# Performance work log

Measured on AMD Instinct MI355X. Metric: run time of the kernel, lower is better.

## Reference

```python
import jax, jax.numpy as jnp
import numpy as np

T, WQ, WS, C, H, W = 2, 75, 25, 640, 10, 10
WAY, SHOT = 5, 5
HID = C // 16
SCALE_VALUE = 30.0
ATTEN_SCALE_VALUE = 50.0
FROM_VALUE = 0.5
VALUE_INTERVAL = 0.3
BN_EPS = 1e-5
NORM_EPS = 1e-12


def _leaky(x):
    return jnp.where(x >= 0, x, 0.2 * x)


def _l2norm(x, axis):
    n = jnp.sqrt(jnp.sum(x * x, axis=axis, keepdims=True))
    return x / jnp.maximum(n, NORM_EPS)


def _embed(x, W_conv, bn_gamma, bn_beta, bn_mean, bn_var):
    # 1x1 conv (no bias) + eval-mode BatchNorm + LeakyReLU(0.2)
    # x: [t, n, c, h, w] -> [t, n, c, h, w]
    y = jnp.einsum('oc,tnchw->tnohw', W_conv, x)
    inv = bn_gamma / jnp.sqrt(bn_var + BN_EPS)
    y = y * inv[:, None, None] + (bn_beta - bn_mean * inv)[:, None, None]
    return _leaky(y)


def setup_inputs() -> dict:
    key = jax.random.key(0)
    ks = jax.random.split(key, 5)
    return {
        'query_feat': jax.random.normal(ks[0], (T, WQ, C, H, W), dtype=jnp.float32),
        'support_feat': jax.random.normal(ks[1], (T, WS, C, H, W), dtype=jnp.float32),
        'W_conv': jax.random.normal(ks[2], (C, C), dtype=jnp.float32) * 0.02,
        'bn_gamma': jnp.ones((C,), jnp.float32),
        'bn_beta': jnp.zeros((C,), jnp.float32),
        'bn_mean': jnp.zeros((C,), jnp.float32),
        'bn_var': jnp.ones((C,), jnp.float32),
        'psi_w1': jax.random.normal(ks[3], (C, HID), dtype=jnp.float32) * 0.04,
        'psi_b1': jnp.zeros((HID,), jnp.float32),
        'psi_w2': jax.random.normal(ks[4], (HID, 1), dtype=jnp.float32) * 0.15,
        'psi_b2': jnp.zeros((1,), jnp.float32),
        'way_num': WAY,
        'shot_num': SHOT,
    }


def reference(query_feat, support_feat, W_conv, bn_gamma, bn_beta, bn_mean, bn_var,
              psi_w1, psi_b1, psi_w2, psi_b2, way_num, shot_num):
    t, wq, c, h, w = query_feat.shape
    ws = support_feat.shape[1]
    hw = h * w

    # embedded + normalized features for the gated branch
    w_query = _embed(query_feat, W_conv, bn_gamma, bn_beta, bn_mean, bn_var)
    w_query = w_query.reshape(t, wq, c, hw).transpose(0, 1, 3, 2)      # [t, wq, hw, c]
    w_support = _embed(support_feat, W_conv, bn_gamma, bn_beta, bn_mean, bn_var)
    w_support = w_support.reshape(t, ws, c, hw).transpose(0, 2, 1, 3).reshape(t, c, ws * hw)
    w_query = _l2norm(w_query, axis=3)
    w_support = _l2norm(w_support, axis=1)

    # cosine similarity of embedded features: [t, wq, hw, ws*hw]
    f_x = jnp.einsum('tqpc,tck->tqpk', w_query, w_support)

    # AEAModule: per-location adaptive threshold from f_psi MLP
    hid = _leaky(w_query @ psi_w1 + psi_b1)                            # [t, wq, hw, HID]
    clamp_value = jax.nn.sigmoid(hid @ psi_w2 + psi_b2) * VALUE_INTERVAL + FROM_VALUE
    clamp_fx = jax.nn.sigmoid(ATTEN_SCALE_VALUE * (f_x - clamp_value))
    atten_score = clamp_fx / jnp.maximum(
        jnp.sum(jnp.abs(clamp_fx), axis=-1, keepdims=True), NORM_EPS)  # L1 normalize

    # raw-feature cosine similarity
    qf = _l2norm(query_feat.reshape(t, wq, c, hw).transpose(0, 1, 3, 2), axis=3)
    sf = _l2norm(support_feat.reshape(t, ws, c, hw).transpose(0, 2, 1, 3).reshape(t, c, ws * hw), axis=1)
    match_score = jnp.einsum('tqpc,tck->tqpk', qf, sf)                 # [t, wq, hw, ws*hw]

    # gate, regroup support axis into (way, shot, hw_s), reduce
    ams = (atten_score * match_score).reshape(t, wq, hw, way_num, shot_num, hw)
    score = ams.sum(axis=-1).mean(axis=(2, 4)) * SCALE_VALUE           # [t, wq, way]
    return score
```

## Files before the change

kernel.cpp:

```cpp
#include <hip/hip_runtime.h>
#include <stdint.h>

#define T_    2
#define WQ_   75
#define WS_   25
#define C_    640
#define HW_   100
#define HID_  40
#define WAY_  5
#define QP_   (WQ_*HW_)
#define SP_   (WS_*HW_)
#define NPT_  60
#define QT_   (NPT_*128)
#define KPAD_ 512
#define KROWS_ (WAY_*KPAD_)
#define C8_   (C_/8)
#define BM_   256
#define BNK_  128

typedef _Float16 f16;
typedef _Float16 f16x8 __attribute__((ext_vector_type(8)));
typedef _Float16 f16x4 __attribute__((ext_vector_type(4)));
typedef _Float16 f16x16 __attribute__((ext_vector_type(16)));
typedef float    f32x4 __attribute__((ext_vector_type(4)));
typedef float    f32x16 __attribute__((ext_vector_type(16)));
typedef uint32_t u32;

__device__ __forceinline__ void gl_lds16(const f16* g, f16* l) {
  __builtin_amdgcn_global_load_lds(
      (const __attribute__((address_space(1))) u32*)g,
      (__attribute__((address_space(3))) u32*)l, 16, 0, 0);
}

#define NB0_ (T_*(WQ_+WS_))
#define KWN_ (C_*C8_ + 48*C8_)
#define NBW_ ((KWN_ + 511)/512)
#define PADN_ (T_*C8_*(QT_-QP_) + T_*C8_*WAY_*12 + T_*(QT_-QP_))
#define NBP_ ((PADN_ + 511)/512)

__global__ __launch_bounds__(512) void ksetup(
    const float* __restrict__ q, const float* __restrict__ s,
    const float* __restrict__ W, const float* __restrict__ w1,
    float* __restrict__ rq_inv, float* __restrict__ rq_nrm,
    float* __restrict__ rs_inv, float* __restrict__ rs_nrm,
    f16* __restrict__ Wr, f16* __restrict__ Wt8, f16* __restrict__ w1t,
    f16* __restrict__ Bq_raw, f16* __restrict__ As_raw) {
  int blk = blockIdx.x;
  int tid = threadIdx.x;

  if (blk < NB0_) {
    __shared__ float part[4][128];
    int t = blk / (WQ_ + WS_);
    int n = blk % (WQ_ + WS_);
    int seg = tid >> 7, p = tid & 127;
    const float* base; float* oi; float* on; size_t idx;
    if (n < WQ_) {
      base = q + ((size_t)(t*WQ_ + n))*C_*HW_;
      idx = (size_t)t*QT_ + n*HW_ + p; oi = rq_inv; on = rq_nrm;
    } else {
      int m = n - WQ_;
      base = s + ((size_t)(t*WS_ + m))*C_*HW_;
      idx = (size_t)t*SP_ + m*HW_ + p; oi = rs_inv; on = rs_nrm;
    }
    float ss = 0.f;
    if (p < HW_) {
      for (int c = seg*160; c < seg*160 + 160; ++c) {
        float v = base[c*HW_ + p]; ss += v*v;
      }
    }
    part[seg][p] = ss;
    __syncthreads();
    if (seg == 0 && p < HW_) {
      float tot = part[0][p] + part[1][p] + part[2][p] + part[3][p];
      float nrm = fmaxf(sqrtf(tot), 1e-12f);
      oi[idx] = 1.f/nrm; on[idx] = nrm;
    }
    return;
  }
  if (blk < NB0_ + NBW_) {
    int idx = (blk - NB0_)*512 + tid;
    if (idx < C_*C8_) {
      int o = idx / C8_, c8 = idx % C8_;
      f16x8 v;
#pragma unroll
      for (int i = 0; i < 8; ++i) v[i] = (f16)W[(size_t)o*C_ + c8*8 + i];
      *reinterpret_cast<f16x8*>(Wr + (size_t)o*C_ + c8*8) = v;
      *reinterpret_cast<f16x8*>(Wt8 + ((size_t)c8*C_ + o)*8) = v;
    } else if (idx < KWN_) {
      int k2 = idx - C_*C8_;
      int h = k2 / C8_, c8 = k2 % C8_;
      f16x8 v;
#pragma unroll
      for (int i = 0; i < 8; ++i)
        v[i] = (h < HID_) ? (f16)w1[(size_t)(c8*8+i)*HID_ + h] : (f16)0.f;
      *reinterpret_cast<f16x8*>(w1t + (size_t)h*C_ + c8*8) = v;
    }
    return;
  }
  {
    int idx = (blk - NB0_ - NBW_)*512 + tid;
    const float4 z4 = make_float4(0.f, 0.f, 0.f, 0.f);
    if (idx < T_*C8_*(QT_-QP_)) {
      int pp = idx % (QT_-QP_); int m = idx / (QT_-QP_);
      int c8 = m % C8_; int t = m / C8_;
      *reinterpret_cast<float4*>(Bq_raw + ((size_t)(t*C8_+c8)*QT_ + QP_ + pp)*8) = z4;
      return;
    }
    int i2 = idx - T_*C8_*(QT_-QP_);
    if (i2 < T_*C8_*WAY_*12) {
      int r = i2 % 12; int m = i2 / 12;
      int wy = m % WAY_; m /= WAY_;
      int c8 = m % C8_; int t = m / C8_;
      *reinterpret_cast<float4*>(
          As_raw + ((size_t)(t*C8_+c8)*KROWS_ + (size_t)wy*KPAD_ + 500 + r)*8) = z4;
      return;
    }
    int i3 = i2 - T_*C8_*WAY_*12;
    if (i3 < T_*(QT_-QP_)) {
      int pp = i3 % (QT_-QP_); int t = i3 / (QT_-QP_);
      rq_inv[(size_t)t*QT_ + QP_ + pp] = 0.f;
      rq_nrm[(size_t)t*QT_ + QP_ + pp] = 0.f;
    }
  }
}

__global__ __launch_bounds__(256) void k1_pack_qraw(
    const float* __restrict__ q, const float* __restrict__ rq_inv,
    f16* __restrict__ Bq_raw) {
  int b = blockIdx.x;
  int ct = b % 10; b /= 10;
  int qq = b % WQ_; int t = b / WQ_;
  int c0 = ct*64;
  __shared__ float lds[64*HW_];
  const float4* s4 = reinterpret_cast<const float4*>(
      q + (((size_t)(t*WQ_ + qq))*C_ + c0)*HW_);
  float4* l4 = reinterpret_cast<float4*>(lds);
  for (int i = threadIdx.x; i < 64*HW_/4; i += 256) l4[i] = s4[i];
  __syncthreads();
  for (int ch = threadIdx.x; ch < 8*HW_; ch += 256) {
    int lc8 = ch / HW_, p = ch % HW_;
    float inv = rq_inv[(size_t)t*QT_ + qq*HW_ + p];
    f16x8 v;
#pragma unroll
    for (int i = 0; i < 8; ++i) v[i] = (f16)(lds[(lc8*8 + i)*HW_ + p] * inv);
    *reinterpret_cast<f16x8*>(
        Bq_raw + ((size_t)(t*C8_ + c0/8 + lc8)*QT_ + qq*HW_ + p)*8) = v;
  }
}

__global__ __launch_bounds__(256) void k2_pack_sraw(
    const float* __restrict__ s, const float* __restrict__ rs_inv,
    f16* __restrict__ As_raw) {
  int b = blockIdx.x;
  int ct = b % 10; b /= 10;
  int n = b % WS_; int t = b / WS_;
  int c0 = ct*64;
  __shared__ float lds[64*HW_];
  const float4* s4 = reinterpret_cast<const float4*>(
      s + (((size_t)(t*WS_ + n))*C_ + c0)*HW_);
  float4* l4 = reinterpret_cast<float4*>(lds);
  for (int i = threadIdx.x; i < 64*HW_/4; i += 256) l4[i] = s4[i];
  __syncthreads();
  for (int ch = threadIdx.x; ch < HW_*8; ch += 256) {
    int p = ch / 8, cc = ch % 8;
    float inv = rs_inv[t*SP_ + n*HW_ + p];
    f16x8 v;
#pragma unroll
    for (int i = 0; i < 8; ++i) v[i] = (f16)(lds[(cc*8 + i)*HW_ + p] * inv);
    int k = n*HW_ + p;
    int way = k / 500, ki = k % 500;
    size_t row = (size_t)way*KPAD_ + ki;
    *reinterpret_cast<f16x8*>(As_raw + ((size_t)(t*C8_ + c0/8 + cc)*KROWS_ + row)*8) = v;
  }
}

__global__ __launch_bounds__(512) void k3_embed_support(
    const f16* __restrict__ As_raw, const f16* __restrict__ Wt8,
    const float* __restrict__ rs_nrm,
    const float* __restrict__ g, const float* __restrict__ be,
    const float* __restrict__ mu, const float* __restrict__ va,
    f16* __restrict__ As_emb) {
  int b = blockIdx.x;
  int t = b / (KROWS_/32);
  int row0 = (b % (KROWS_/32)) * 32;
  int tid = threadIdx.x, wv = tid >> 6, lane = tid & 63;
  int mf = wv & 1, nh = wv >> 1;
  __shared__ f16 Alds[32*32];
  __shared__ f16 Blds[32*C_];
  __shared__ float rowss[32];
  f32x4 acc[10];
#pragma unroll
  for (int i = 0; i < 10; ++i) acc[i] = (f32x4){0.f,0.f,0.f,0.f};

  for (int cs = 0; cs < 20; ++cs) {
    if (tid < 128) {
      int c8l = tid >> 5, r = tid & 31;
      *reinterpret_cast<f16x8*>(Alds + (c8l*32 + r)*8) =
        *reinterpret_cast<const f16x8*>(
            As_raw + ((size_t)(t*C8_ + cs*4 + c8l)*KROWS_ + row0 + r)*8);
    }
    const f16x8* bsrc = reinterpret_cast<const f16x8*>(Wt8 + (size_t)(cs*4)*C_*8);
    f16x8* bdst = reinterpret_cast<f16x8*>(Blds);
    for (int i = tid; i < 4*C_; i += 512) bdst[i] = bsrc[i];
    __syncthreads();
    f16x8 a = *reinterpret_cast<const f16x8*>(
        Alds + ((lane>>4)*32 + mf*16 + (lane&15))*8);
#pragma unroll
    for (int nf = 0; nf < 10; ++nf) {
      int o = nh*160 + nf*16 + (lane & 15);
      f16x8 bf = *reinterpret_cast<const f16x8*>(Blds + (((lane>>4)*C_) + o)*8);
      acc[nf] = __builtin_amdgcn_mfma_f32_16x16x32_f16(a, bf, acc[nf], 0, 0, 0);
    }
    __syncthreads();
  }

  if (tid < 32) rowss[tid] = 0.f;
  __syncthreads();
  int rg = lane >> 4, cl = lane & 15;
  int lrow = mf*16 + rg*4;
  int prow = row0 + lrow;
#pragma unroll
  for (int j = 0; j < 4; ++j) {
    int pr = prow + j;
    int way = pr / KPAD_, ki = pr - way*KPAD_;
    bool valid = ki < 500;
    float nrm = valid ? rs_nrm[t*SP_ + way*500 + ki] : 0.f;
    float ssum = 0.f;
#pragma unroll
    for (int nf = 0; nf < 10; ++nf) {
      int o = nh*160 + nf*16 + cl;
      float inv = g[o] / sqrtf(va[o] + 1e-5f);
      float sh = be[o] - mu[o]*inv;
      float y = acc[nf][j]*nrm*inv + sh;
      y = (y >= 0.f) ? y : 0.2f*y;
      if (!valid) y = 0.f;
      acc[nf][j] = y;
      ssum += y*y;
    }
#pragma unroll
    for (int m = 1; m < 16; m <<= 1) ssum += __shfl_xor(ssum, m);
    if (cl == 0) atomicAdd(&rowss[lrow + j], ssum);
  }
  __syncthreads();
#pragma unroll
  for (int j = 0; j < 4; ++j) {
    int pr = prow + j;
    float invn = 1.f / fmaxf(sqrtf(rowss[lrow + j]), 1e-12f);
#pragma unroll
    for (int nf = 0; nf < 10; ++nf) {
      int o = nh*160 + nf*16 + cl;
      As_emb[((size_t)(t*C8_ + (o>>3))*KROWS_ + pr)*8 + (o&7)] = (f16)(acc[nf][j]*invn);
    }
  }
}

__global__ __launch_bounds__(256, 3) void k4_embed_query(
    const f16* __restrict__ Wr, const f16* __restrict__ Bq_raw,
    const float* __restrict__ rq_nrm,
    const float* __restrict__ g, const float* __restrict__ be,
    const float* __restrict__ mu, const float* __restrict__ va,
    f16* __restrict__ Bq_emb) {
  __shared__ f16 Ab[3][128*32];
  __shared__ f16 Bb[3][4*128*8];
  int b = blockIdx.x;
  int ot = b % 5; int m = b / 5;
  int pt = m % NPT_; int t = m / NPT_;
  int o0 = ot*128;
  int tid = threadIdx.x, w = tid >> 6, lane = tid & 63;
  int la_r = lane >> 2, la_c = lane & 3;

  auto stage = [&](int buf, int cs) {
#pragma unroll
    for (int i = 0; i < 2; ++i) {
      int ca = w*2 + i;
      int r = ca*16 + la_r;
      int sc = la_c ^ (r & 3);
      gl_lds16(Wr + (size_t)(o0 + r)*C_ + cs*32 + sc*8, &Ab[buf][ca*512]);
    }
#pragma unroll
    for (int i = 0; i < 2; ++i) {
      int cb = w*2 + i;
      int c8l = cb >> 1;
      size_t src = ((size_t)(t*C8_ + cs*4 + c8l)*QT_ + pt*128 + (cb&1)*64 + lane)*8;
      gl_lds16(Bq_raw + src, &Bb[buf][(c8l*128 + (cb&1)*64)*8]);
    }
  };

  f32x4 acc[2][8];
#pragma unroll
  for (int a = 0; a < 2; ++a)
#pragma unroll
    for (int n = 0; n < 8; ++n) acc[a][n] = (f32x4){0.f,0.f,0.f,0.f};

  stage(0, 0);
  stage(1, 1);
  for (int cs = 0; cs < 20; ++cs) {
    int buf = cs % 3;
    if (cs < 19) asm volatile("s_waitcnt vmcnt(4)" ::: "memory");
    else         asm volatile("s_waitcnt vmcnt(0)" ::: "memory");
    __builtin_amdgcn_s_barrier();
    if (cs < 18) stage((cs+2)%3, cs+2);
    __builtin_amdgcn_s_setprio(1);
    f16x8 fa[2];
#pragma unroll
    for (int mi = 0; mi < 2; ++mi) {
      int R = w*32 + mi*16 + (lane & 15);
      int sc = (lane >> 4) ^ (R & 3);
      fa[mi] = *reinterpret_cast<const f16x8*>(&Ab[buf][R*32 + sc*8]);
    }
#pragma unroll
    for (int nf = 0; nf < 8; ++nf) {
      f16x8 fb = *reinterpret_cast<const f16x8*>(
          &Bb[buf][((lane>>4)*128 + nf*16 + (lane&15))*8]);
#pragma unroll
      for (int mi = 0; mi < 2; ++mi)
        acc[mi][nf] = __builtin_amdgcn_mfma_f32_16x16x32_f16(fa[mi], fb, acc[mi][nf], 0, 0, 0);
    }
    __builtin_amdgcn_s_setprio(0);
  }

#pragma unroll
  for (int mi = 0; mi < 2; ++mi) {
    int obase = o0 + w*32 + mi*16 + (lane>>4)*4;
    float inv4[4], sh4[4];
#pragma unroll
    for (int j = 0; j < 4; ++j) {
      int o = obase + j;
      inv4[j] = g[o] / sqrtf(va[o] + 1e-5f);
      sh4[j] = be[o] - mu[o]*inv4[j];
    }
#pragma unroll
    for (int nf = 0; nf < 8; ++nf) {
      size_t gp = (size_t)pt*128 + nf*16 + (lane & 15);
      float nrmv = rq_nrm[(size_t)t*QT_ + gp];
      f16x4 vv;
#pragma unroll
      for (int j = 0; j < 4; ++j) {
        float y = (nrmv > 0.f) ? (acc[mi][nf][j]*nrmv*inv4[j] + sh4[j]) : 0.f;
        y = (y >= 0.f) ? y : 0.2f*y;
        vv[j] = (f16)y;
      }
      *reinterpret_cast<f16x4*>(
          &Bq_emb[((size_t)(t*C8_ + (obase>>3))*QT_ + gp)*8 + (obase&7)]) = vv;
    }
  }
}

__global__ __launch_bounds__(256) void k5_colnorm_psi(
    const f16* __restrict__ Bq_emb, const f16* __restrict__ w1t,
    const float* __restrict__ b1, const float* __restrict__ w2,
    const float* __restrict__ b2, float* __restrict__ cv,
    float* __restrict__ invq) {
  __shared__ float ssA[2][128];
  __shared__ float invs[128];
  __shared__ float hidL[48*128];
  int bq = blockIdx.x;
  int pt = bq % NPT_, t = bq / NPT_;
  int tid = threadIdx.x, w = tid >> 6, lane = tid & 63;
  size_t pbase = (size_t)pt*128;

  auto bptr = [&](int c8, int pp) -> const f16* {
    return Bq_emb + ((size_t)(t*C8_ + c8)*QT_ + pbase + pp)*8;
  };

  {
    int h2 = tid >> 7, pp = tid & 127;
    float ss = 0.f;
    for (int c8 = h2*40; c8 < h2*40 + 40; ++c8) {
      f16x8 v = *reinterpret_cast<const f16x8*>(bptr(c8, pp));
#pragma unroll
      for (int i = 0; i < 8; ++i) { float x = (float)v[i]; ss += x*x; }
    }
    ssA[h2][pp] = ss;
  }
  for (int i = tid; i < 48*128; i += 256) hidL[i] = 0.f;
  __syncthreads();
  if (tid < 128) {
    float ss = ssA[0][tid] + ssA[1][tid];
    float inv = (ss > 0.f) ? (1.f / fmaxf(sqrtf(ss), 1e-12f)) : 0.f;
    invs[tid] = inv;
    invq[(size_t)t*QT_ + pbase + tid] = inv;
  }

  f32x4 acc[3][8];
#pragma unroll
  for (int a = 0; a < 3; ++a)
#pragma unroll
    for (int n = 0; n < 8; ++n) acc[a][n] = (f32x4){0.f,0.f,0.f,0.f};
  for (int r = 0; r < 5; ++r) {
    int cs = w + r*4;
    f16x8 fa[3];
#pragma unroll
    for (int mf = 0; mf < 3; ++mf) {
      int R = mf*16 + (lane & 15);
      fa[mf] = *reinterpret_cast<const f16x8*>(&w1t[(size_t)R*C_ + cs*32 + (lane>>4)*8]);
    }
#pragma unroll
    for (int nf = 0; nf < 8; ++nf) {
      f16x8 fb = *reinterpret_cast<const f16x8*>(
          bptr(cs*4 + (lane>>4), nf*16 + (lane&15)));
#pragma unroll
      for (int mf = 0; mf < 3; ++mf)
        acc[mf][nf] = __builtin_amdgcn_mfma_f32_16x16x32_f16(fa[mf], fb, acc[mf][nf], 0, 0, 0);
    }
  }
  __syncthreads();
  for (int rr = 0; rr < 4; ++rr) {
    if (w == rr) {
#pragma unroll
      for (int mf = 0; mf < 3; ++mf)
#pragma unroll
        for (int nf = 0; nf < 8; ++nf)
#pragma unroll
          for (int j = 0; j < 4; ++j) {
            int row = mf*16 + (lane>>4)*4 + j;
            int col = nf*16 + (lane & 15);
            hidL[row*128 + col] += acc[mf][nf][j];
          }
    }
    __syncthreads();
  }
  if (tid < 128) {
    float inv = invs[tid];
    float z = b2[0];
    for (int h = 0; h < HID_; ++h) {
      float hv = hidL[h*128 + tid]*inv + b1[h];
      hv = (hv >= 0.f) ? hv : 0.2f*hv;
      z += hv*w2[h];
    }
    cv[(size_t)t*QT_ + pbase + tid] = 0.3f/(1.f + __expf(-z)) + 0.5f;
  }
}

__global__ __launch_bounds__(256, 2) void k6_main(
    const f16* __restrict__ As_emb, const f16* __restrict__ As_raw,
    const f16* __restrict__ Bq_emb, const f16* __restrict__ Bq_raw,
    const float* __restrict__ cv, const float* __restrict__ invq,
    float* __restrict__ Spart, float* __restrict__ L1part) {
  __shared__ f16 Ab[3][4*BM_*8];
  __shared__ f16 Bb[3][4*BNK_*8];
  __shared__ float cvs[BNK_], iqs[BNK_], Ss[BNK_], L1s[BNK_];

  int bid = blockIdx.x;
  int l = (bid & 7)*150 + (bid >> 3);
  int wk = l % 10; int m = l / 10;
  int pt = m % NPT_; int t = m / NPT_;
  int way = wk >> 1, kt = wk & 1;

  int tid = threadIdx.x, w = tid >> 6, lane = tid & 63;
  if (tid < BNK_) {
    cvs[tid] = cv[(size_t)t*QT_ + pt*128 + tid];
    iqs[tid] = invq[(size_t)t*QT_ + pt*128 + tid];
    Ss[tid] = 0.f; L1s[tid] = 0.f;
  }
  int wrow0 = w*64;
  size_t rowb = (size_t)way*KPAD_ + (size_t)kt*BM_;

  const size_t aoff = ((size_t)(t*C8_ + w)*KROWS_ + rowb + lane)*8;
  const size_t boff = ((size_t)(t*C8_ + w)*QT_ + (size_t)pt*128 + lane)*8;
  const f16* pA = As_raw + aoff;
  const f16* pB = Bq_raw + boff;
  const f16* pA1 = As_emb + aoff;
  const f16* pB1 = Bq_emb + boff;
  const int CS_A = 4*KROWS_*8;
  const int CS_B = 4*QT_*8;

  auto stage = [&](int buf, const f16* a, const f16* bsrc) {
    f16* da = &Ab[buf][(size_t)w*BM_*8];
    f16* db = &Bb[buf][(size_t)w*BNK_*8];
    gl_lds16(a,        da);
    gl_lds16(a + 512,  da + 512);
    gl_lds16(a + 1024, da + 1024);
    gl_lds16(a + 1536, da + 1536);
    gl_lds16(bsrc,       db);
    gl_lds16(bsrc + 512, db + 512);
  };

  f32x16 acc[2][4];
  f16x16 mtc[2][4];
#pragma unroll
  for (int mi = 0; mi < 2; ++mi)
#pragma unroll
    for (int nf = 0; nf < 4; ++nf) acc[mi][nf] = (f32x16)(0.f);
  float Sl[4] = {0,0,0,0}, L1l[4] = {0,0,0,0};

  stage(0, pA, pB); pA += CS_A; pB += CS_B;
  stage(1, pA, pB); pA += CS_A; pB += CS_B;

  for (int ph = 0; ph < 40; ++ph) {
    if (ph == 18) { pA = pA1; pB = pB1; }
    int buf = ph % 3;
    if (ph < 39) asm volatile("s_waitcnt vmcnt(6)" ::: "memory");
    else         asm volatile("s_waitcnt vmcnt(0)" ::: "memory");
    __builtin_amdgcn_s_barrier();
    if (ph < 38) { stage((ph+2)%3, pA, pB); pA += CS_A; pB += CS_B; }
    __builtin_amdgcn_s_setprio(1);
    const f16* Abuf = Ab[buf];
    const f16* Bbuf = Bb[buf];
    int r0 = wrow0 + (lane & 31);
#pragma unroll
    for (int ks = 0; ks < 2; ++ks) {
      int c8l = ks*2 + (lane >> 5);
      f16x8 fa0 = *reinterpret_cast<const f16x8*>(&Abuf[(c8l*BM_ + r0)*8]);
      f16x8 fa1 = *reinterpret_cast<const f16x8*>(&Abuf[(c8l*BM_ + r0 + 32)*8]);
#pragma unroll
      for (int nf = 0; nf < 4; ++nf) {
        f16x8 fb = *reinterpret_cast<const f16x8*>(
            &Bbuf[(c8l*BNK_ + nf*32 + (lane & 31))*8]);
        acc[0][nf] = __builtin_amdgcn_mfma_f32_32x32x16_f16(fa0, fb, acc[0][nf], 0, 0, 0);
        acc[1][nf] = __builtin_amdgcn_mfma_f32_32x32x16_f16(fa1, fb, acc[1][nf], 0, 0, 0);
      }
    }
    __builtin_amdgcn_s_setprio(0);

    if (ph == 19) {
#pragma unroll
      for (int mi = 0; mi < 2; ++mi)
#pragma unroll
        for (int nf = 0; nf < 4; ++nf)
#pragma unroll
          for (int jj = 0; jj < 16; ++jj) {
            mtc[mi][nf][jj] = (f16)fminf(fmaxf(acc[mi][nf][jj], -8.f), 8.f);
            acc[mi][nf][jj] = 0.f;
          }
    } else if (ph == 39) {
#pragma unroll
      for (int nf = 0; nf < 4; ++nf) {
        int col = nf*32 + (lane & 31);
        float cvv = cvs[col];
        float iq = iqs[col];
#pragma unroll
        for (int mi = 0; mi < 2; ++mi)
#pragma unroll
          for (int jj = 0; jj < 16; ++jj) {
            float fx = acc[mi][nf][jj] * iq;
            float sg = 1.f/(1.f + __expf(-50.f*(fx - cvv)));
            Sl[nf]  += sg * (float)mtc[mi][nf][jj];
            L1l[nf] += sg;
          }
      }
    }
  }

#pragma unroll
  for (int nf = 0; nf < 4; ++nf) {
    float vs = Sl[nf] + __shfl_xor(Sl[nf], 32);
    float vl = L1l[nf] + __shfl_xor(L1l[nf], 32);
    if (lane < 32) {
      atomicAdd(&Ss[nf*32 + lane], vs);
      atomicAdd(&L1s[nf*32 + lane], vl);
    }
  }
  __syncthreads();
  if (tid < BNK_) {
    size_t o = ((size_t)((t*WAY_ + way)*2 + kt))*QT_ + (size_t)pt*128 + tid;
    Spart[o] = Ss[tid]; L1part[o] = L1s[tid];
  }
}

__global__ __launch_bounds__(128) void k7_reduce(
    const float* __restrict__ Spart, const float* __restrict__ L1part,
    float* __restrict__ out) {
  int b = blockIdx.x;
  int t = b / WQ_, q = b % WQ_;
  int tid = threadIdx.x;
  __shared__ float red[128];
  float contrib[WAY_] = {0,0,0,0,0};
  if (tid < HW_) {
    size_t p = (size_t)q*HW_ + tid;
    float l1 = 0.f;
#pragma unroll
    for (int w = 0; w < WAY_; ++w)
#pragma unroll
      for (int k = 0; k < 2; ++k)
        l1 += L1part[((size_t)((t*WAY_ + w)*2 + k))*QT_ + p];
    l1 = fmaxf(l1, 1e-12f);
#pragma unroll
    for (int w = 0; w < WAY_; ++w) {
      float sv = 0.f;
#pragma unroll
      for (int k = 0; k < 2; ++k)
        sv += Spart[((size_t)((t*WAY_ + w)*2 + k))*QT_ + p];
      contrib[w] = sv / l1;
    }
  }
#pragma unroll
  for (int w = 0; w < WAY_; ++w) {
    red[tid] = contrib[w];
    __syncthreads();
    for (int off = 64; off > 0; off >>= 1) {
      if (tid < off) red[tid] += red[tid + off];
      __syncthreads();
    }
    if (tid == 0) out[b*WAY_ + w] = red[0] * 30.f / (float)(HW_*5);
    __syncthreads();
  }
}

extern "C" void kernel_launch(void* const* d_in, const int* in_sizes, int n_in,
                              void* d_out, int out_size, void* d_ws, size_t ws_size,
                              hipStream_t stream) {
  (void)in_sizes; (void)n_in; (void)out_size; (void)ws_size;
  const float* q  = (const float*)d_in[0];
  const float* s  = (const float*)d_in[1];
  const float* W  = (const float*)d_in[2];
  const float* g  = (const float*)d_in[3];
  const float* be = (const float*)d_in[4];
  const float* mu = (const float*)d_in[5];
  const float* va = (const float*)d_in[6];
  const float* w1 = (const float*)d_in[7];
  const float* b1 = (const float*)d_in[8];
  const float* w2 = (const float*)d_in[9];
  const float* b2 = (const float*)d_in[10];
  float* out = (float*)d_out;
  char* ws = (char*)d_ws;

  size_t off = 0;
  auto nxt = [&](size_t bytes) { size_t o = off; off += (bytes + 255) & ~(size_t)255; return o; };
  float* rq_inv = (float*)(ws + nxt((size_t)T_*QT_*4));
  float* rq_nrm = (float*)(ws + nxt((size_t)T_*QT_*4));
  float* rs_inv = (float*)(ws + nxt((size_t)T_*SP_*4));
  float* rs_nrm = (float*)(ws + nxt((size_t)T_*SP_*4));
  f16* Wr     = (f16*)(ws + nxt((size_t)C_*C_*2));
  f16* Wt8    = (f16*)(ws + nxt((size_t)C_*C_*2));
  f16* w1t    = (f16*)(ws + nxt((size_t)48*C_*2));
  f16* As_raw = (f16*)(ws + nxt((size_t)T_*KROWS_*C_*2));
  f16* As_emb = (f16*)(ws + nxt((size_t)T_*KROWS_*C_*2));
  f16* Bq_raw = (f16*)(ws + nxt((size_t)T_*C8_*QT_*8*2));
  f16* Bq_emb = (f16*)(ws + nxt((size_t)T_*C8_*QT_*8*2));
  float* cvp    = (float*)(ws + nxt((size_t)T_*QT_*4));
  float* invq   = (float*)(ws + nxt((size_t)T_*QT_*4));
  float* Spart  = (float*)(ws + nxt((size_t)T_*WAY_*2*QT_*4));
  float* L1part = (float*)(ws + nxt((size_t)T_*WAY_*2*QT_*4));

  ksetup<<<NB0_ + NBW_ + NBP_, 512, 0, stream>>>(
      q, s, W, w1, rq_inv, rq_nrm, rs_inv, rs_nrm, Wr, Wt8, w1t, Bq_raw, As_raw);
  k1_pack_qraw<<<T_*WQ_*10, 256, 0, stream>>>(q, rq_inv, Bq_raw);
  k2_pack_sraw<<<T_*WS_*10, 256, 0, stream>>>(s, rs_inv, As_raw);
  k3_embed_support<<<T_*(KROWS_/32), 512, 0, stream>>>(As_raw, Wt8, rs_nrm, g, be, mu, va, As_emb);
  k4_embed_query<<<T_*5*NPT_, 256, 0, stream>>>(Wr, Bq_raw, rq_nrm, g, be, mu, va, Bq_emb);
  k5_colnorm_psi<<<T_*NPT_, 256, 0, stream>>>(Bq_emb, w1t, b1, w2, b2, cvp, invq);
  k6_main<<<1200, 256, 0, stream>>>(As_emb, As_raw, Bq_emb, Bq_raw, cvp, invq, Spart, L1part);
  k7_reduce<<<T_*WQ_, 128, 0, stream>>>(Spart, L1part, out);
}
```

Baseline: 283.7 us.

## Split k6 tile across eight waves with redistributed LDS staging

The main similarity kernel now runs 512 threads (8 waves) per block instead of 4, with each wave computing 32 rows of the 256x128 tile instead of 64. Global-to-LDS staging is spread so each wave issues three 16-byte loads per stage, and the wait count drops to match. This halves per-wave accumulators and is meant to raise latency hiding. In exchange, each wave reuses every B fragment for half as many MFMAs, which doubles LDS B reads per flop. The `__launch_bounds__(512, 4)` request forces a very tight VGPR budget that risks register spills, and the LDS footprint probably caps residency at two blocks regardless.

```diff
diff --git a/kernel.cpp b/kernel.cpp
--- a/kernel.cpp
+++ b/kernel.cpp
@@ -432,7 +432,7 @@
   }
 }
 
-__global__ __launch_bounds__(256, 2) void k6_main(
+__global__ __launch_bounds__(512, 4) void k6_main(
     const f16* __restrict__ As_emb, const f16* __restrict__ As_raw,
     const f16* __restrict__ Bq_emb, const f16* __restrict__ Bq_raw,
     const float* __restrict__ cv, const float* __restrict__ invq,
@@ -453,11 +453,11 @@
     iqs[tid] = invq[(size_t)t*QT_ + pt*128 + tid];
     Ss[tid] = 0.f; L1s[tid] = 0.f;
   }
-  int wrow0 = w*64;
+  int wrow0 = w*32;
   size_t rowb = (size_t)way*KPAD_ + (size_t)kt*BM_;
 
-  const size_t aoff = ((size_t)(t*C8_ + w)*KROWS_ + rowb + lane)*8;
-  const size_t boff = ((size_t)(t*C8_ + w)*QT_ + (size_t)pt*128 + lane)*8;
+  const size_t aoff = ((size_t)t*C8_*KROWS_ + rowb + lane)*8;
+  const size_t boff = ((size_t)t*C8_*QT_ + (size_t)pt*128 + lane)*8;
   const f16* pA = As_raw + aoff;
   const f16* pB = Bq_raw + boff;
   const f16* pA1 = As_emb + aoff;
@@ -465,23 +465,23 @@
   const int CS_A = 4*KROWS_*8;
   const int CS_B = 4*QT_*8;
 
-  auto stage = [&](int buf, const f16* a, const f16* bsrc) {
-    f16* da = &Ab[buf][(size_t)w*BM_*8];
-    f16* db = &Bb[buf][(size_t)w*BNK_*8];
-    gl_lds16(a,        da);
-    gl_lds16(a + 512,  da + 512);
-    gl_lds16(a + 1024, da + 1024);
-    gl_lds16(a + 1536, da + 1536);
-    gl_lds16(bsrc,       db);
-    gl_lds16(bsrc + 512, db + 512);
+  auto stage = [&](int buf, const f16* baseA, const f16* baseB) {
+#pragma unroll
+    for (int i = 0; i < 3; ++i) {
+      int c = 3*w + i;
+      if (c < 16) {
+        gl_lds16(baseA + ((size_t)(c>>2)*KROWS_ + (c&3)*64)*8, &Ab[buf][c*512]);
+      } else {
+        int cb = c - 16;
+        gl_lds16(baseB + ((size_t)(cb>>1)*QT_ + (cb&1)*64)*8, &Bb[buf][cb*512]);
+      }
+    }
   };
 
-  f32x16 acc[2][4];
-  f16x16 mtc[2][4];
-#pragma unroll
-  for (int mi = 0; mi < 2; ++mi)
-#pragma unroll
-    for (int nf = 0; nf < 4; ++nf) acc[mi][nf] = (f32x16)(0.f);
+  f32x16 acc[4];
+  f16x16 mtc[4];
+#pragma unroll
+  for (int nf = 0; nf < 4; ++nf) acc[nf] = (f32x16)(0.f);
   float Sl[4] = {0,0,0,0}, L1l[4] = {0,0,0,0};
 
   stage(0, pA, pB); pA += CS_A; pB += CS_B;
@@ -490,7 +490,7 @@
   for (int ph = 0; ph < 40; ++ph) {
     if (ph == 18) { pA = pA1; pB = pB1; }
     int buf = ph % 3;
-    if (ph < 39) asm volatile("s_waitcnt vmcnt(6)" ::: "memory");
+    if (ph < 39) asm volatile("s_waitcnt vmcnt(3)" ::: "memory");
     else         asm volatile("s_waitcnt vmcnt(0)" ::: "memory");
     __builtin_amdgcn_s_barrier();
     if (ph < 38) { stage((ph+2)%3, pA, pB); pA += CS_A; pB += CS_B; }
@@ -501,28 +501,24 @@
 #pragma unroll
     for (int ks = 0; ks < 2; ++ks) {
       int c8l = ks*2 + (lane >> 5);
-      f16x8 fa0 = *reinterpret_cast<const f16x8*>(&Abuf[(c8l*BM_ + r0)*8]);
-      f16x8 fa1 = *reinterpret_cast<const f16x8*>(&Abuf[(c8l*BM_ + r0 + 32)*8]);
+      f16x8 fa = *reinterpret_cast<const f16x8*>(&Abuf[(c8l*BM_ + r0)*8]);
 #pragma unroll
       for (int nf = 0; nf < 4; ++nf) {
         f16x8 fb = *reinterpret_cast<const f16x8*>(
             &Bbuf[(c8l*BNK_ + nf*32 + (lane & 31))*8]);
-        acc[0][nf] = __builtin_amdgcn_mfma_f32_32x32x16_f16(fa0, fb, acc[0][nf], 0, 0, 0);
-        acc[1][nf] = __builtin_amdgcn_mfma_f32_32x32x16_f16(fa1, fb, acc[1][nf], 0, 0, 0);
+        acc[nf] = __builtin_amdgcn_mfma_f32_32x32x16_f16(fa, fb, acc[nf], 0, 0, 0);
       }
     }
     __builtin_amdgcn_s_setprio(0);
 
     if (ph == 19) {
 #pragma unroll
-      for (int mi = 0; mi < 2; ++mi)
-#pragma unroll
-        for (int nf = 0; nf < 4; ++nf)
-#pragma unroll
-          for (int jj = 0; jj < 16; ++jj) {
-            mtc[mi][nf][jj] = (f16)fminf(fmaxf(acc[mi][nf][jj], -8.f), 8.f);
-            acc[mi][nf][jj] = 0.f;
-          }
+      for (int nf = 0; nf < 4; ++nf)
+#pragma unroll
+        for (int jj = 0; jj < 16; ++jj) {
+          mtc[nf][jj] = (f16)fminf(fmaxf(acc[nf][jj], -8.f), 8.f);
+          acc[nf][jj] = 0.f;
+        }
     } else if (ph == 39) {
 #pragma unroll
       for (int nf = 0; nf < 4; ++nf) {
@@ -530,14 +526,12 @@
         float cvv = cvs[col];
         float iq = iqs[col];
 #pragma unroll
-        for (int mi = 0; mi < 2; ++mi)
-#pragma unroll
-          for (int jj = 0; jj < 16; ++jj) {
-            float fx = acc[mi][nf][jj] * iq;
-            float sg = 1.f/(1.f + __expf(-50.f*(fx - cvv)));
-            Sl[nf]  += sg * (float)mtc[mi][nf][jj];
-            L1l[nf] += sg;
-          }
+        for (int jj = 0; jj < 16; ++jj) {
+          float fx = acc[nf][jj] * iq;
+          float sg = 1.f/(1.f + __expf(-50.f*(fx - cvv)));
+          Sl[nf]  += sg * (float)mtc[nf][jj];
+          L1l[nf] += sg;
+        }
       }
     }
   }
@@ -640,6 +634,6 @@
   k3_embed_support<<<T_*(KROWS_/32), 512, 0, stream>>>(As_raw, Wt8, rs_nrm, g, be, mu, va, As_emb);
   k4_embed_query<<<T_*5*NPT_, 256, 0, stream>>>(Wr, Bq_raw, rq_nrm, g, be, mu, va, Bq_emb);
   k5_colnorm_psi<<<T_*NPT_, 256, 0, stream>>>(Bq_emb, w1t, b1, w2, b2, cvp, invq);
-  k6_main<<<1200, 256, 0, stream>>>(As_emb, As_raw, Bq_emb, Bq_raw, cvp, invq, Spart, L1part);
+  k6_main<<<1200, 512, 0, stream>>>(As_emb, As_raw, Bq_emb, Bq_raw, cvp, invq, Spart, L1part);
   k7_reduce<<<T_*WQ_, 128, 0, stream>>>(Spart, L1part, out);
 }
```

Result: slower. 338.0 us (+19.1%).
